# Kernel optimization log

Measured on AMD Instinct MI355X. Metric: run time of the kernel, lower is better.

The kernel has to match this reference:

```python
import jax, jax.numpy as jnp
import numpy as np

S = 2048      # seq_len
H = 32        # num_heads
G = 8         # num_groups (KV heads)
D = 128       # head_dim
HPG = H // G  # heads per group
MODEL = H * D


def setup_inputs() -> dict:
    rng = jax.random.key(0)
    ks = jax.random.split(rng, 6)
    return {
        "query": jax.random.normal(ks[0], (S, H, D), jnp.float32),
        "key":   jax.random.normal(ks[1], (S, G, D), jnp.float32),
        "value": jax.random.normal(ks[2], (S, G, D), jnp.float32),
        "mask":  jnp.zeros((S, S), jnp.float32),
        "w_out": jax.random.normal(ks[3], (MODEL, MODEL), jnp.float32) * (MODEL ** -0.5),
        "b_out": jnp.zeros((MODEL,), jnp.float32),
    }


def reference(query, key, value, mask, w_out, b_out):
    # NOTE: the original torch module prepares `mask` but never applies it to
    # the attention scores; we faithfully reproduce that (mask is unused).
    scale = D ** -0.5
    # [S,H,D] -> [H,S,D] -> [G,HPG,S,D]; head h = g*HPG + i (torch .view split)
    q = query.transpose(1, 0, 2).reshape(G, HPG, S, D)
    k = key.transpose(1, 0, 2)    # [G,S,D]
    v = value.transpose(1, 0, 2)  # [G,S,D]
    scores = jnp.einsum('ghqd,gkd->ghqk', q, k) * scale  # [G,HPG,S,S]
    attn = jax.nn.softmax(scores, axis=-1)
    out = jnp.einsum('ghqk,gkd->ghqd', attn, v)          # [G,HPG,S,D]
    # [G,HPG,S,D] -> [H,S,D] -> [S,H,D] -> [S, H*D]
    out = out.reshape(H, S, D).transpose(1, 0, 2).reshape(S, MODEL)
    out = out @ w_out.T + b_out                           # out_proj (Linear)
    return out.reshape(S, H, D)
```

## Files before the change

kernel.cpp:

```cpp
#include <hip/hip_runtime.h>
#include <hip/hip_bf16.h>
#include <stdint.h>

constexpr int S_ = 2048, H_ = 32, G_ = 8, HPG_ = 4, D_ = 128, MODEL_ = 4096;

typedef __attribute__((ext_vector_type(4))) float f32x4;
typedef __attribute__((ext_vector_type(16))) float f32x16;
typedef __attribute__((ext_vector_type(8))) short bf16x8;
typedef __attribute__((ext_vector_type(4))) short bf16x4;

__device__ inline unsigned short f2bf(float f) {
  unsigned u = __float_as_uint(f);
  u += 0x7FFFu + ((u >> 16) & 1u);
  return (unsigned short)(u >> 16);
}

__device__ inline unsigned cvt_pk_bf16(float lo, float hi) {
  unsigned r;
  asm("v_cvt_pk_bf16_f32 %0, %1, %2" : "=v"(r) : "v"(lo), "v"(hi));
  return r;
}

__device__ inline void gload_lds16(const void* g, void* l) {
  __builtin_amdgcn_global_load_lds(
      (const __attribute__((address_space(1))) unsigned int*)g,
      (__attribute__((address_space(3))) unsigned int*)l,
      16, 0, 0);
}

__global__ __launch_bounds__(256) void cvt_f32_to_bf16(
    const float* __restrict__ in, unsigned short* __restrict__ out, int n4) {
  int i = blockIdx.x * 256 + threadIdx.x;
  if (i < n4) {
    float4 v = reinterpret_cast<const float4*>(in)[i];
    bf16x4 o;
    o[0] = f2bf(v.x); o[1] = f2bf(v.y); o[2] = f2bf(v.z); o[3] = f2bf(v.w);
    reinterpret_cast<bf16x4*>(out)[i] = o;
  }
}

__global__ __launch_bounds__(256) void cvt_k_kernel(
    const float* __restrict__ in, unsigned short* __restrict__ out) {
  int i = blockIdx.x * 256 + threadIdx.x;
  int d4 = i & 31, g = (i >> 5) & 7, s = i >> 8;
  float4 v = reinterpret_cast<const float4*>(in)[i];
  bf16x4 o;
  o[0] = f2bf(v.x); o[1] = f2bf(v.y); o[2] = f2bf(v.z); o[3] = f2bf(v.w);
  reinterpret_cast<bf16x4*>(out)[(g * S_ + s) * 32 + d4] = o;
}

__global__ __launch_bounds__(256) void cvt_v_kernel(
    const float* __restrict__ in, unsigned short* __restrict__ out) {
  __shared__ float t[64][33];
  int s0 = blockIdx.x * 64, d0 = blockIdx.y * 32, g = blockIdx.z;
  int tid = threadIdx.x;
#pragma unroll
  for (int p = 0; p < 2; ++p) {
    int idx = p * 256 + tid;
    int s = idx >> 3, dq = (idx & 7) * 4;
    float4 v = *reinterpret_cast<const float4*>(
        in + ((size_t)(s0 + s) * G_ + g) * D_ + d0 + dq);
    t[s][dq] = v.x; t[s][dq + 1] = v.y; t[s][dq + 2] = v.z; t[s][dq + 3] = v.w;
  }
  __syncthreads();
  int d = tid >> 3, sq = (tid & 7) * 8;
  bf16x8 o;
#pragma unroll
  for (int j = 0; j < 8; ++j) o[j] = f2bf(t[sq + j][d]);
  *reinterpret_cast<bf16x8*>(out + ((size_t)g * D_ + d0 + d) * S_ + s0 + sq) = o;
}

constexpr int QB2 = 128, KVB = 32, NT = S_ / KVB;
constexpr float RTHR = 8.0f;

__global__ __launch_bounds__(256, 2) void attn32_kernel(
    const float* __restrict__ q, const unsigned short* __restrict__ kb,
    const unsigned short* __restrict__ vtb, unsigned short* __restrict__ aout) {
  __shared__ __align__(16) char smem[65536];

  const int qt = blockIdx.x, h = blockIdx.y;
  const int g = h >> 2;
  const int tid = threadIdx.x, w = tid >> 6, lane = tid & 63;
  const int l31 = lane & 31, hi = lane >> 5;

  const float scale2 = 0.12751742354783493f;
  bf16x8 qf[8];
  const int qrow = qt * QB2 + w * 32 + l31;
  {
    const float* qp = q + ((size_t)qrow * H_ + h) * D_;
#pragma unroll
    for (int c = 0; c < 8; ++c) {
      const float* p0 = qp + c * 16 + hi * 8;
      float4 a = *(const float4*)p0;
      float4 b = *(const float4*)(p0 + 4);
      bf16x8 f;
      f[0] = f2bf(a.x * scale2); f[1] = f2bf(a.y * scale2);
      f[2] = f2bf(a.z * scale2); f[3] = f2bf(a.w * scale2);
      f[4] = f2bf(b.x * scale2); f[5] = f2bf(b.y * scale2);
      f[6] = f2bf(b.z * scale2); f[7] = f2bf(b.w * scale2);
      qf[c] = f;
    }
  }

  int ks_kv[2], ks_d[2], vs_d[2], vs_kv[2];
#pragma unroll
  for (int hh = 0; hh < 2; ++hh) {
    int p = w * 1024 + hh * 4096 + lane * 16;
    int kvr = p >> 8;
    ks_kv[hh] = kvr;
    ks_d[hh] = ((p & 255) ^ ((kvr & 7) << 4)) >> 1;
    int dr = p >> 6;
    vs_d[hh] = dr;
    vs_kv[hh] = ((p & 63) ^ (((dr >> 1) & 3) << 4)) >> 1;
  }
  const unsigned short* kg = kb + (size_t)g * S_ * D_;
  const unsigned short* vg = vtb + (size_t)g * D_ * S_;

  auto stage = [&](int t) {
    int kv0 = t * KVB;
    char* Kd = smem + (t & 3) * 16384;
    char* Vd = Kd + 8192;
#pragma unroll
    for (int hh = 0; hh < 2; ++hh) {
      gload_lds16(kg + (size_t)(kv0 + ks_kv[hh]) * D_ + ks_d[hh],
                  Kd + w * 1024 + hh * 4096);
      gload_lds16(vg + (size_t)vs_d[hh] * S_ + kv0 + vs_kv[hh],
                  Vd + w * 1024 + hh * 4096);
    }
  };

  f32x16 of[4];
#pragma unroll
  for (int i = 0; i < 4; ++i) of[i] = (f32x16)0.f;
  float m = -1e30f, l = 0.f;

  auto process = [&](int t) {
    const char* Kd = smem + (t & 3) * 16384;
    const char* Vd = Kd + 8192;

    f32x16 s0 = (f32x16)0.f, s1 = (f32x16)0.f;
    __builtin_amdgcn_s_setprio(1);
#pragma unroll
    for (int c = 0; c < 8; ++c) {
      unsigned off = ((unsigned)(l31 * 256 + c * 32 + hi * 16)) ^
                     ((unsigned)(l31 & 7) << 4);
      bf16x8 kf = *(const bf16x8*)(Kd + off);
      if (c & 1)
        s1 = __builtin_amdgcn_mfma_f32_32x32x16_bf16(kf, qf[c], s1, 0, 0, 0);
      else
        s0 = __builtin_amdgcn_mfma_f32_32x32x16_bf16(kf, qf[c], s0, 0, 0, 0);
    }
    __builtin_amdgcn_s_setprio(0);
    f32x16 sv = s0 + s1;

    float mx8[8];
#pragma unroll
    for (int i = 0; i < 8; ++i) mx8[i] = fmaxf(sv[i], sv[i + 8]);
#pragma unroll
    for (int i = 0; i < 4; ++i) mx8[i] = fmaxf(mx8[i], mx8[i + 4]);
    float tmax = fmaxf(fmaxf(mx8[0], mx8[1]), fmaxf(mx8[2], mx8[3]));
    tmax = fmaxf(tmax, __shfl_xor(tmax, 32));
    if (__any(tmax > m + RTHR)) {
      float mnew = fmaxf(m, tmax);
      float alpha = __builtin_exp2f(m - mnew);
#pragma unroll
      for (int i = 0; i < 4; ++i)
#pragma unroll
        for (int r = 0; r < 16; ++r) of[i][r] *= alpha;
      l *= alpha;
      m = mnew;
    }
    float pv[16], ps[8];
#pragma unroll
    for (int r = 0; r < 16; ++r) pv[r] = __builtin_exp2f(sv[r] - m);
#pragma unroll
    for (int i = 0; i < 8; ++i) ps[i] = pv[i] + pv[i + 8];
#pragma unroll
    for (int i = 0; i < 4; ++i) ps[i] += ps[i + 4];
    float sum = (ps[0] + ps[1]) + (ps[2] + ps[3]);
    sum += __shfl_xor(sum, 32);
    l += sum;

    unsigned pk[8];
#pragma unroll
    for (int b = 0; b < 8; ++b) pk[b] = cvt_pk_bf16(pv[2 * b], pv[2 * b + 1]);
    bf16x8 pf[2];
#pragma unroll
    for (int kc = 0; kc < 2; ++kc) {
      auto sA = __builtin_amdgcn_permlane32_swap(pk[kc * 4 + 0], pk[kc * 4 + 2],
                                                 false, false);
      auto sB = __builtin_amdgcn_permlane32_swap(pk[kc * 4 + 1], pk[kc * 4 + 3],
                                                 false, false);
      unsigned fr[4] = {(unsigned)sA[0], (unsigned)sB[0],
                        (unsigned)sA[1], (unsigned)sB[1]};
      __builtin_memcpy(&pf[kc], fr, 16);
    }

    __builtin_amdgcn_s_setprio(1);
#pragma unroll
    for (int db = 0; db < 4; ++db) {
      int d = db * 32 + l31;
#pragma unroll
      for (int kc = 0; kc < 2; ++kc) {
        unsigned off = ((unsigned)(d * 64 + kc * 32 + hi * 16)) ^
                       ((unsigned)((d >> 1) & 3) << 4);
        bf16x8 vf = *(const bf16x8*)(Vd + off);
        of[db] = __builtin_amdgcn_mfma_f32_32x32x16_bf16(vf, pf[kc], of[db], 0, 0, 0);
      }
    }
    __builtin_amdgcn_s_setprio(0);
  };

  stage(0); stage(1);
  asm volatile("s_waitcnt vmcnt(0)" ::: "memory");
  __builtin_amdgcn_s_barrier();
  stage(2); stage(3);

  for (int t = 0; t < NT; t += 2) {
    process(t);
    process(t + 1);
    asm volatile("s_waitcnt vmcnt(0)" ::: "memory");
    __builtin_amdgcn_s_barrier();
    if (t + 4 < NT) { stage(t + 4); stage(t + 5); }
  }

  __syncthreads();
  float inv = 1.0f / l;
  unsigned short* Ol = (unsigned short*)smem;
  const int ql = w * 32 + l31;
#pragma unroll
  for (int db = 0; db < 4; ++db) {
#pragma unroll
    for (int rp = 0; rp < 8; ++rp) {
      int r0 = rp * 2;
      int d0 = db * 32 + (r0 & 3) + 8 * (r0 >> 2) + 4 * hi;
      unsigned pkv = cvt_pk_bf16(of[db][r0] * inv, of[db][r0 + 1] * inv);
      unsigned off = ((unsigned)(ql * 256 + d0 * 2)) ^ ((unsigned)(ql & 7) << 4);
      *(unsigned*)((char*)Ol + off) = pkv;
    }
  }
  __syncthreads();
  const size_t obase = ((size_t)qt * QB2) * MODEL_ + (size_t)h * D_;
#pragma unroll
  for (int pass = 0; pass < 8; ++pass) {
    int row = pass * 16 + (tid >> 4);
    int c = tid & 15;
    unsigned off = ((unsigned)(row * 256 + c * 16)) ^ ((unsigned)(row & 7) << 4);
    bf16x8 vv = *(const bf16x8*)((char*)Ol + off);
    *(bf16x8*)(aout + obase + (size_t)row * MODEL_ + c * 8) = vv;
  }
}

constexpr int BM = 128, BN = 128, BK = 64;

__global__ __launch_bounds__(256, 2) void gemm_bt_bias(
    const unsigned short* __restrict__ A, const unsigned short* __restrict__ B,
    const float* __restrict__ bias, float* __restrict__ C) {
  __shared__ unsigned short As[BM * BK];
  __shared__ unsigned short Bs[BN * BK];

  const int tid = threadIdx.x;
  const int w = tid >> 6, lane = tid & 63;
  const int wr = w >> 1, wc = w & 1;
  const int r16 = lane & 15, g4 = lane >> 4;
  const int row0 = blockIdx.y * BM, col0 = blockIdx.x * BN;

  f32x4 acc[4][4];
#pragma unroll
  for (int m = 0; m < 4; ++m)
#pragma unroll
    for (int n = 0; n < 4; ++n) acc[m][n] = (f32x4)0.f;

  for (int kt = 0; kt < MODEL_ / BK; ++kt) {
    const int k0 = kt * BK;
    __syncthreads();
#pragma unroll
    for (int j = 0; j < 4; ++j) {
      int chunk = w * 4 + j;
      int sb = chunk * 1024 + lane * 16;
      int srow = sb >> 7;
      int lb = sb ^ ((srow & 7) << 4);
      int kk = (lb & 127) >> 1;
      gload_lds16(A + (size_t)(row0 + srow) * MODEL_ + k0 + kk,
                  (char*)As + chunk * 1024);
      gload_lds16(B + (size_t)(col0 + srow) * MODEL_ + k0 + kk,
                  (char*)Bs + chunk * 1024);
    }
    asm volatile("s_waitcnt vmcnt(0)" ::: "memory");
    __syncthreads();

#pragma unroll
    for (int kc = 0; kc < 2; ++kc) {
      bf16x8 af[4], bfr[4];
#pragma unroll
      for (int m = 0; m < 4; ++m) {
        int row = wr * 64 + m * 16 + r16;
        unsigned off = ((unsigned)(row * 128 + (kc * 32 + g4 * 8) * 2)) ^ ((row & 7) << 4);
        af[m] = *(bf16x8*)((char*)As + off);
      }
#pragma unroll
      for (int n = 0; n < 4; ++n) {
        int row = wc * 64 + n * 16 + r16;
        unsigned off = ((unsigned)(row * 128 + (kc * 32 + g4 * 8) * 2)) ^ ((row & 7) << 4);
        bfr[n] = *(bf16x8*)((char*)Bs + off);
      }
#pragma unroll
      for (int m = 0; m < 4; ++m)
#pragma unroll
        for (int n = 0; n < 4; ++n)
          acc[m][n] = __builtin_amdgcn_mfma_f32_16x16x32_bf16(af[m], bfr[n], acc[m][n], 0, 0, 0);
    }
  }

#pragma unroll
  for (int n = 0; n < 4; ++n) {
    int col = col0 + wc * 64 + n * 16 + r16;
    float bv = bias[col];
#pragma unroll
    for (int m = 0; m < 4; ++m) {
      int rbase = row0 + wr * 64 + m * 16 + g4 * 4;
#pragma unroll
      for (int j = 0; j < 4; ++j)
        C[(size_t)(rbase + j) * MODEL_ + col] = acc[m][n][j] + bv;
    }
  }
}

extern "C" void kernel_launch(void* const* d_in, const int* in_sizes, int n_in,
                              void* d_out, int out_size, void* d_ws, size_t ws_size,
                              hipStream_t stream) {
  const float* q = (const float*)d_in[0];
  const float* k = (const float*)d_in[1];
  const float* v = (const float*)d_in[2];
  const float* w_out = (const float*)d_in[4];
  const float* b_out = (const float*)d_in[5];
  float* out = (float*)d_out;

  unsigned short* attn_bf = (unsigned short*)d_ws;
  unsigned short* xreg = attn_bf + (size_t)S_ * MODEL_;
  unsigned short* k_bf = xreg;
  unsigned short* vt_bf = xreg + (size_t)G_ * S_ * D_;
  unsigned short* w_bf = xreg;
  if (ws_size < ((size_t)S_ * MODEL_ + (size_t)MODEL_ * MODEL_) * 2) return;

  cvt_k_kernel<<<S_ * G_ * D_ / 4 / 256, 256, 0, stream>>>(k, k_bf);
  dim3 vg(S_ / 64, D_ / 32, G_);
  cvt_v_kernel<<<vg, 256, 0, stream>>>(v, vt_bf);

  dim3 ag(S_ / QB2, H_);
  attn32_kernel<<<ag, 256, 0, stream>>>(q, k_bf, vt_bf, attn_bf);

  cvt_f32_to_bf16<<<(MODEL_ * MODEL_ / 4) / 256, 256, 0, stream>>>(
      w_out, w_bf, MODEL_ * MODEL_ / 4);

  dim3 gg(MODEL_ / BN, S_ / BM);
  gemm_bt_bias<<<gg, 256, 0, stream>>>(attn_bf, w_bf, b_out, out);
}
```

Measured before the change: 190.5 us.

## Widen attention KV tile to 64 with double-buffered LDS stages

Raises the KV block per iteration from 32 to 64 keys. Each step now does two score MFMA chains and four PV MFMAs, with a single online-softmax max/rescale check per 64 keys instead of per 32. The LDS layout and XOR swizzles are reworked for 256-byte K rows and 128-byte V^T rows, and the four-slot ring becomes two 32KB buffers. This halves the per-tile softmax and reduction overhead but uses more registers per step and keeps the same total LDS prefetch depth.

Result: slower. 198.1 us (+4.0%).

```diff
diff --git a/kernel.cpp b/kernel.cpp
--- a/kernel.cpp
+++ b/kernel.cpp
@@ -70,7 +70,7 @@
   *reinterpret_cast<bf16x8*>(out + ((size_t)g * D_ + d0 + d) * S_ + s0 + sq) = o;
 }
 
-constexpr int QB2 = 128, KVB = 32, NT = S_ / KVB;
+constexpr int QB2 = 128, KVB = 64, NT2 = S_ / KVB;
 constexpr float RTHR = 8.0f;
 
 __global__ __launch_bounds__(256, 2) void attn32_kernel(
@@ -102,30 +102,30 @@
     }
   }
 
-  int ks_kv[2], ks_d[2], vs_d[2], vs_kv[2];
-#pragma unroll
-  for (int hh = 0; hh < 2; ++hh) {
-    int p = w * 1024 + hh * 4096 + lane * 16;
+  int ks_kv[4], ks_d[4], vs_d[4], vs_kv[4];
+#pragma unroll
+  for (int it = 0; it < 4; ++it) {
+    int p = it * 4096 + w * 1024 + lane * 16;
     int kvr = p >> 8;
-    ks_kv[hh] = kvr;
-    ks_d[hh] = ((p & 255) ^ ((kvr & 7) << 4)) >> 1;
-    int dr = p >> 6;
-    vs_d[hh] = dr;
-    vs_kv[hh] = ((p & 63) ^ (((dr >> 1) & 3) << 4)) >> 1;
+    ks_kv[it] = kvr;
+    ks_d[it] = ((p & 255) ^ ((kvr & 15) << 4)) >> 1;
+    int dr = p >> 7;
+    vs_d[it] = dr;
+    vs_kv[it] = ((p & 127) ^ ((dr & 7) << 4)) >> 1;
   }
   const unsigned short* kg = kb + (size_t)g * S_ * D_;
   const unsigned short* vg = vtb + (size_t)g * D_ * S_;
 
   auto stage = [&](int t) {
     int kv0 = t * KVB;
-    char* Kd = smem + (t & 3) * 16384;
-    char* Vd = Kd + 8192;
-#pragma unroll
-    for (int hh = 0; hh < 2; ++hh) {
-      gload_lds16(kg + (size_t)(kv0 + ks_kv[hh]) * D_ + ks_d[hh],
-                  Kd + w * 1024 + hh * 4096);
-      gload_lds16(vg + (size_t)vs_d[hh] * S_ + kv0 + vs_kv[hh],
-                  Vd + w * 1024 + hh * 4096);
+    char* Kd = smem + (t & 1) * 32768;
+    char* Vd = Kd + 16384;
+#pragma unroll
+    for (int it = 0; it < 4; ++it) {
+      gload_lds16(kg + (size_t)(kv0 + ks_kv[it]) * D_ + ks_d[it],
+                  Kd + it * 4096 + w * 1024);
+      gload_lds16(vg + (size_t)vs_d[it] * S_ + kv0 + vs_kv[it],
+                  Vd + it * 4096 + w * 1024);
     }
   };
 
@@ -135,30 +135,39 @@
   float m = -1e30f, l = 0.f;
 
   auto process = [&](int t) {
-    const char* Kd = smem + (t & 3) * 16384;
-    const char* Vd = Kd + 8192;
+    const char* Kd = smem + (t & 1) * 32768;
+    const char* Vd = Kd + 16384;
 
     f32x16 s0 = (f32x16)0.f, s1 = (f32x16)0.f;
+    f32x16 s2 = (f32x16)0.f, s3 = (f32x16)0.f;
     __builtin_amdgcn_s_setprio(1);
 #pragma unroll
     for (int c = 0; c < 8; ++c) {
-      unsigned off = ((unsigned)(l31 * 256 + c * 32 + hi * 16)) ^
-                     ((unsigned)(l31 & 7) << 4);
-      bf16x8 kf = *(const bf16x8*)(Kd + off);
-      if (c & 1)
-        s1 = __builtin_amdgcn_mfma_f32_32x32x16_bf16(kf, qf[c], s1, 0, 0, 0);
-      else
-        s0 = __builtin_amdgcn_mfma_f32_32x32x16_bf16(kf, qf[c], s0, 0, 0, 0);
+      unsigned off0 = ((unsigned)(l31 * 256 + c * 32 + hi * 16)) ^
+                      ((unsigned)(l31 & 15) << 4);
+      unsigned off1 = ((unsigned)((32 + l31) * 256 + c * 32 + hi * 16)) ^
+                      ((unsigned)(l31 & 15) << 4);
+      bf16x8 kf0 = *(const bf16x8*)(Kd + off0);
+      bf16x8 kf1 = *(const bf16x8*)(Kd + off1);
+      if (c & 1) {
+        s1 = __builtin_amdgcn_mfma_f32_32x32x16_bf16(kf0, qf[c], s1, 0, 0, 0);
+        s3 = __builtin_amdgcn_mfma_f32_32x32x16_bf16(kf1, qf[c], s3, 0, 0, 0);
+      } else {
+        s0 = __builtin_amdgcn_mfma_f32_32x32x16_bf16(kf0, qf[c], s0, 0, 0, 0);
+        s2 = __builtin_amdgcn_mfma_f32_32x32x16_bf16(kf1, qf[c], s2, 0, 0, 0);
+      }
     }
     __builtin_amdgcn_s_setprio(0);
-    f32x16 sv = s0 + s1;
-
-    float mx8[8];
-#pragma unroll
-    for (int i = 0; i < 8; ++i) mx8[i] = fmaxf(sv[i], sv[i + 8]);
-#pragma unroll
-    for (int i = 0; i < 4; ++i) mx8[i] = fmaxf(mx8[i], mx8[i + 4]);
-    float tmax = fmaxf(fmaxf(mx8[0], mx8[1]), fmaxf(mx8[2], mx8[3]));
+    f32x16 sv0 = s0 + s1, sv1 = s2 + s3;
+
+    float mx[16];
+#pragma unroll
+    for (int i = 0; i < 16; ++i) mx[i] = fmaxf(sv0[i], sv1[i]);
+#pragma unroll
+    for (int i = 0; i < 8; ++i) mx[i] = fmaxf(mx[i], mx[i + 8]);
+#pragma unroll
+    for (int i = 0; i < 4; ++i) mx[i] = fmaxf(mx[i], mx[i + 4]);
+    float tmax = fmaxf(fmaxf(mx[0], mx[1]), fmaxf(mx[2], mx[3]));
     tmax = fmaxf(tmax, __shfl_xor(tmax, 32));
     if (__any(tmax > m + RTHR)) {
       float mnew = fmaxf(m, tmax);
@@ -170,30 +179,38 @@
       l *= alpha;
       m = mnew;
     }
-    float pv[16], ps[8];
-#pragma unroll
-    for (int r = 0; r < 16; ++r) pv[r] = __builtin_exp2f(sv[r] - m);
-#pragma unroll
-    for (int i = 0; i < 8; ++i) ps[i] = pv[i] + pv[i + 8];
+    float pv0[16], pv1[16], ps[16];
+#pragma unroll
+    for (int r = 0; r < 16; ++r) pv0[r] = __builtin_exp2f(sv0[r] - m);
+#pragma unroll
+    for (int r = 0; r < 16; ++r) pv1[r] = __builtin_exp2f(sv1[r] - m);
+#pragma unroll
+    for (int i = 0; i < 16; ++i) ps[i] = pv0[i] + pv1[i];
+#pragma unroll
+    for (int i = 0; i < 8; ++i) ps[i] += ps[i + 8];
 #pragma unroll
     for (int i = 0; i < 4; ++i) ps[i] += ps[i + 4];
     float sum = (ps[0] + ps[1]) + (ps[2] + ps[3]);
     sum += __shfl_xor(sum, 32);
     l += sum;
 
-    unsigned pk[8];
-#pragma unroll
-    for (int b = 0; b < 8; ++b) pk[b] = cvt_pk_bf16(pv[2 * b], pv[2 * b + 1]);
-    bf16x8 pf[2];
-#pragma unroll
-    for (int kc = 0; kc < 2; ++kc) {
-      auto sA = __builtin_amdgcn_permlane32_swap(pk[kc * 4 + 0], pk[kc * 4 + 2],
-                                                 false, false);
-      auto sB = __builtin_amdgcn_permlane32_swap(pk[kc * 4 + 1], pk[kc * 4 + 3],
-                                                 false, false);
-      unsigned fr[4] = {(unsigned)sA[0], (unsigned)sB[0],
-                        (unsigned)sA[1], (unsigned)sB[1]};
-      __builtin_memcpy(&pf[kc], fr, 16);
+    bf16x8 pf[4];
+#pragma unroll
+    for (int sl = 0; sl < 2; ++sl) {
+      const float* pp = sl ? pv1 : pv0;
+      unsigned pk[8];
+#pragma unroll
+      for (int b = 0; b < 8; ++b) pk[b] = cvt_pk_bf16(pp[2 * b], pp[2 * b + 1]);
+#pragma unroll
+      for (int kc = 0; kc < 2; ++kc) {
+        auto sA = __builtin_amdgcn_permlane32_swap(pk[kc * 4 + 0], pk[kc * 4 + 2],
+                                                   false, false);
+        auto sB = __builtin_amdgcn_permlane32_swap(pk[kc * 4 + 1], pk[kc * 4 + 3],
+                                                   false, false);
+        unsigned fr[4] = {(unsigned)sA[0], (unsigned)sB[0],
+                          (unsigned)sA[1], (unsigned)sB[1]};
+        __builtin_memcpy(&pf[sl * 2 + kc], fr, 16);
+      }
     }
 
     __builtin_amdgcn_s_setprio(1);
@@ -201,9 +218,9 @@
     for (int db = 0; db < 4; ++db) {
       int d = db * 32 + l31;
 #pragma unroll
-      for (int kc = 0; kc < 2; ++kc) {
-        unsigned off = ((unsigned)(d * 64 + kc * 32 + hi * 16)) ^
-                       ((unsigned)((d >> 1) & 3) << 4);
+      for (int kc = 0; kc < 4; ++kc) {
+        unsigned off = ((unsigned)(d * 128 + kc * 32 + hi * 16)) ^
+                       ((unsigned)(d & 7) << 4);
         bf16x8 vf = *(const bf16x8*)(Vd + off);
         of[db] = __builtin_amdgcn_mfma_f32_32x32x16_bf16(vf, pf[kc], of[db], 0, 0, 0);
       }
@@ -211,17 +228,16 @@
     __builtin_amdgcn_s_setprio(0);
   };
 
-  stage(0); stage(1);
+  stage(0);
   asm volatile("s_waitcnt vmcnt(0)" ::: "memory");
   __builtin_amdgcn_s_barrier();
-  stage(2); stage(3);
-
-  for (int t = 0; t < NT; t += 2) {
+  stage(1);
+
+  for (int t = 0; t < NT2; ++t) {
     process(t);
-    process(t + 1);
     asm volatile("s_waitcnt vmcnt(0)" ::: "memory");
     __builtin_amdgcn_s_barrier();
-    if (t + 4 < NT) { stage(t + 4); stage(t + 5); }
+    if (t + 2 < NT2) stage(t + 2);
   }
 
   __syncthreads();
```

## Split attention KV range across two wave groups and merge partial softmax

Applied to the files above, without the earlier changes.

Each attention block now runs 512 threads, with two groups of four waves each processing half of the KV sequence for the same 128 query rows. The partial outputs and running max/sum are merged through shared memory at the end. Staging also drops from a 4-deep to a 2-deep buffer per group, with new LDS swizzles for K and V and a single MFMA accumulator chain. The aim is more waves in flight per CU to hide latency. In exchange it pays for a final merge with extra barriers and LDS traffic, and launch_bounds(512,4) may put pressure on registers.

Result: slower. 281.2 us (+47.6%).

```diff
diff --git a/kernel.cpp b/kernel.cpp
--- a/kernel.cpp
+++ b/kernel.cpp
@@ -70,23 +70,24 @@
   *reinterpret_cast<bf16x8*>(out + ((size_t)g * D_ + d0 + d) * S_ + s0 + sq) = o;
 }
 
-constexpr int QB2 = 128, KVB = 32, NT = S_ / KVB;
+constexpr int QB2 = 128, KVB = 32, NTG = 1024 / KVB;
 constexpr float RTHR = 8.0f;
 
-__global__ __launch_bounds__(256, 2) void attn32_kernel(
+__global__ __launch_bounds__(512, 4) void attn32_kernel(
     const float* __restrict__ q, const unsigned short* __restrict__ kb,
     const unsigned short* __restrict__ vtb, unsigned short* __restrict__ aout) {
-  __shared__ __align__(16) char smem[65536];
+  __shared__ __align__(16) char smem[66560];
 
   const int qt = blockIdx.x, h = blockIdx.y;
   const int g = h >> 2;
   const int tid = threadIdx.x, w = tid >> 6, lane = tid & 63;
   const int l31 = lane & 31, hi = lane >> 5;
+  const int gsel = w >> 2, wq = w & 3;
 
   const float scale2 = 0.12751742354783493f;
   bf16x8 qf[8];
-  const int qrow = qt * QB2 + w * 32 + l31;
   {
+    const int qrow = qt * QB2 + wq * 32 + l31;
     const float* qp = q + ((size_t)qrow * H_ + h) * D_;
 #pragma unroll
     for (int c = 0; c < 8; ++c) {
@@ -102,30 +103,31 @@
     }
   }
 
-  int ks_kv[2], ks_d[2], vs_d[2], vs_kv[2];
-#pragma unroll
-  for (int hh = 0; hh < 2; ++hh) {
-    int p = w * 1024 + hh * 4096 + lane * 16;
+  int kvK[2], dK[2], dV[2], kvV[2];
+#pragma unroll
+  for (int j = 0; j < 2; ++j) {
+    int p = (wq * 2 + j) * 1024 + lane * 16;
     int kvr = p >> 8;
-    ks_kv[hh] = kvr;
-    ks_d[hh] = ((p & 255) ^ ((kvr & 7) << 4)) >> 1;
-    int dr = p >> 6;
-    vs_d[hh] = dr;
-    vs_kv[hh] = ((p & 63) ^ (((dr >> 1) & 3) << 4)) >> 1;
+    kvK[j] = kvr;
+    dK[j] = ((p & 255) ^ ((kvr & 15) << 4)) >> 1;
+    int R = p >> 8;
+    int il = (p & 255) ^ ((R & 7) << 4);
+    dV[j] = R * 4 + (il >> 6);
+    kvV[j] = (il & 63) >> 1;
   }
   const unsigned short* kg = kb + (size_t)g * S_ * D_;
   const unsigned short* vg = vtb + (size_t)g * D_ * S_;
+  const int kvbase = gsel * 1024;
 
   auto stage = [&](int t) {
-    int kv0 = t * KVB;
-    char* Kd = smem + (t & 3) * 16384;
-    char* Vd = Kd + 8192;
-#pragma unroll
-    for (int hh = 0; hh < 2; ++hh) {
-      gload_lds16(kg + (size_t)(kv0 + ks_kv[hh]) * D_ + ks_d[hh],
-                  Kd + w * 1024 + hh * 4096);
-      gload_lds16(vg + (size_t)vs_d[hh] * S_ + kv0 + vs_kv[hh],
-                  Vd + w * 1024 + hh * 4096);
+    int kv0 = kvbase + t * KVB;
+    char* base = smem + (gsel * 2 + (t & 1)) * 16384;
+#pragma unroll
+    for (int j = 0; j < 2; ++j) {
+      gload_lds16(kg + (size_t)(kv0 + kvK[j]) * D_ + dK[j],
+                  base + (wq * 2 + j) * 1024);
+      gload_lds16(vg + (size_t)dV[j] * S_ + kv0 + kvV[j],
+                  base + 8192 + (wq * 2 + j) * 1024);
     }
   };
 
@@ -134,31 +136,33 @@
   for (int i = 0; i < 4; ++i) of[i] = (f32x16)0.f;
   float m = -1e30f, l = 0.f;
 
-  auto process = [&](int t) {
-    const char* Kd = smem + (t & 3) * 16384;
+  stage(0);
+  asm volatile("s_waitcnt vmcnt(0)" ::: "memory");
+  __builtin_amdgcn_s_barrier();
+
+  for (int t = 0; t < NTG; ++t) {
+    if (t + 1 < NTG) stage(t + 1);
+
+    const char* Kd = smem + (gsel * 2 + (t & 1)) * 16384;
     const char* Vd = Kd + 8192;
 
-    f32x16 s0 = (f32x16)0.f, s1 = (f32x16)0.f;
+    f32x16 sv = (f32x16)0.f;
     __builtin_amdgcn_s_setprio(1);
 #pragma unroll
     for (int c = 0; c < 8; ++c) {
-      unsigned off = ((unsigned)(l31 * 256 + c * 32 + hi * 16)) ^
-                     ((unsigned)(l31 & 7) << 4);
+      unsigned off = (unsigned)(l31 * 256) +
+                     (((unsigned)(c * 32 + hi * 16)) ^ ((unsigned)(l31 & 15) << 4));
       bf16x8 kf = *(const bf16x8*)(Kd + off);
-      if (c & 1)
-        s1 = __builtin_amdgcn_mfma_f32_32x32x16_bf16(kf, qf[c], s1, 0, 0, 0);
-      else
-        s0 = __builtin_amdgcn_mfma_f32_32x32x16_bf16(kf, qf[c], s0, 0, 0, 0);
+      sv = __builtin_amdgcn_mfma_f32_32x32x16_bf16(kf, qf[c], sv, 0, 0, 0);
     }
     __builtin_amdgcn_s_setprio(0);
-    f32x16 sv = s0 + s1;
-
-    float mx8[8];
-#pragma unroll
-    for (int i = 0; i < 8; ++i) mx8[i] = fmaxf(sv[i], sv[i + 8]);
-#pragma unroll
-    for (int i = 0; i < 4; ++i) mx8[i] = fmaxf(mx8[i], mx8[i + 4]);
-    float tmax = fmaxf(fmaxf(mx8[0], mx8[1]), fmaxf(mx8[2], mx8[3]));
+
+    float mx[8];
+#pragma unroll
+    for (int i = 0; i < 8; ++i) mx[i] = fmaxf(sv[i], sv[i + 8]);
+#pragma unroll
+    for (int i = 0; i < 4; ++i) mx[i] = fmaxf(mx[i], mx[i + 4]);
+    float tmax = fmaxf(fmaxf(mx[0], mx[1]), fmaxf(mx[2], mx[3]));
     tmax = fmaxf(tmax, __shfl_xor(tmax, 32));
     if (__any(tmax > m + RTHR)) {
       float mnew = fmaxf(m, tmax);
@@ -199,51 +203,72 @@
     __builtin_amdgcn_s_setprio(1);
 #pragma unroll
     for (int db = 0; db < 4; ++db) {
-      int d = db * 32 + l31;
+      int R = db * 8 + (l31 >> 2);
+      unsigned lg = (unsigned)((l31 & 3) * 64);
 #pragma unroll
       for (int kc = 0; kc < 2; ++kc) {
-        unsigned off = ((unsigned)(d * 64 + kc * 32 + hi * 16)) ^
-                       ((unsigned)((d >> 1) & 3) << 4);
+        unsigned off = (unsigned)(R * 256) +
+                       ((lg + (unsigned)(kc * 32 + hi * 16)) ^ ((unsigned)(R & 7) << 4));
         bf16x8 vf = *(const bf16x8*)(Vd + off);
         of[db] = __builtin_amdgcn_mfma_f32_32x32x16_bf16(vf, pf[kc], of[db], 0, 0, 0);
       }
     }
     __builtin_amdgcn_s_setprio(0);
-  };
-
-  stage(0); stage(1);
-  asm volatile("s_waitcnt vmcnt(0)" ::: "memory");
-  __builtin_amdgcn_s_barrier();
-  stage(2); stage(3);
-
-  for (int t = 0; t < NT; t += 2) {
-    process(t);
-    process(t + 1);
+
     asm volatile("s_waitcnt vmcnt(0)" ::: "memory");
     __builtin_amdgcn_s_barrier();
-    if (t + 4 < NT) { stage(t + 4); stage(t + 5); }
-  }
-
+  }
+
+  float* O1 = (float*)smem;
+  float* ml = (float*)(smem + 65536);
+  if (w >= 4) {
+    float* reg = O1 + (w - 4) * 4096;
+#pragma unroll
+    for (int db = 0; db < 4; ++db)
+#pragma unroll
+      for (int r = 0; r < 16; ++r) {
+        int dd = db * 32 + (r & 3) + 8 * (r >> 2) + 4 * hi;
+        reg[dd * 32 + l31] = of[db][r];
+      }
+    if (!hi) { ml[wq * 64 + l31 * 2] = m; ml[wq * 64 + l31 * 2 + 1] = l; }
+  }
   __syncthreads();
-  float inv = 1.0f / l;
+  float inv = 0.f;
+  if (w < 4) {
+    float m1 = ml[wq * 64 + l31 * 2], l1 = ml[wq * 64 + l31 * 2 + 1];
+    float mf = fmaxf(m, m1);
+    float a0 = __builtin_exp2f(m - mf), a1 = __builtin_exp2f(m1 - mf);
+    inv = 1.0f / (l * a0 + l1 * a1);
+    const float* reg = O1 + wq * 4096;
+#pragma unroll
+    for (int db = 0; db < 4; ++db)
+#pragma unroll
+      for (int r = 0; r < 16; ++r) {
+        int dd = db * 32 + (r & 3) + 8 * (r >> 2) + 4 * hi;
+        of[db][r] = of[db][r] * a0 + reg[dd * 32 + l31] * a1;
+      }
+  }
+  __syncthreads();
+
   unsigned short* Ol = (unsigned short*)smem;
-  const int ql = w * 32 + l31;
-#pragma unroll
-  for (int db = 0; db < 4; ++db) {
-#pragma unroll
-    for (int rp = 0; rp < 8; ++rp) {
-      int r0 = rp * 2;
-      int d0 = db * 32 + (r0 & 3) + 8 * (r0 >> 2) + 4 * hi;
-      unsigned pkv = cvt_pk_bf16(of[db][r0] * inv, of[db][r0 + 1] * inv);
-      unsigned off = ((unsigned)(ql * 256 + d0 * 2)) ^ ((unsigned)(ql & 7) << 4);
-      *(unsigned*)((char*)Ol + off) = pkv;
-    }
+  if (w < 4) {
+    const int ql = wq * 32 + l31;
+#pragma unroll
+    for (int db = 0; db < 4; ++db)
+#pragma unroll
+      for (int rp = 0; rp < 8; ++rp) {
+        int r0 = rp * 2;
+        int d0 = db * 32 + (r0 & 3) + 8 * (r0 >> 2) + 4 * hi;
+        unsigned pkv = cvt_pk_bf16(of[db][r0] * inv, of[db][r0 + 1] * inv);
+        unsigned off = ((unsigned)(ql * 256 + d0 * 2)) ^ ((unsigned)(ql & 7) << 4);
+        *(unsigned*)((char*)Ol + off) = pkv;
+      }
   }
   __syncthreads();
   const size_t obase = ((size_t)qt * QB2) * MODEL_ + (size_t)h * D_;
 #pragma unroll
-  for (int pass = 0; pass < 8; ++pass) {
-    int row = pass * 16 + (tid >> 4);
+  for (int pass = 0; pass < 4; ++pass) {
+    int row = pass * 32 + (tid >> 4);
     int c = tid & 15;
     unsigned off = ((unsigned)(row * 256 + c * 16)) ^ ((unsigned)(row & 7) << 4);
     bf16x8 vv = *(const bf16x8*)((char*)Ol + off);
@@ -348,7 +373,7 @@
   cvt_v_kernel<<<vg, 256, 0, stream>>>(v, vt_bf);
 
   dim3 ag(S_ / QB2, H_);
-  attn32_kernel<<<ag, 256, 0, stream>>>(q, k_bf, vt_bf, attn_bf);
+  attn32_kernel<<<ag, 512, 0, stream>>>(q, k_bf, vt_bf, attn_bf);
 
   cvt_f32_to_bf16<<<(MODEL_ * MODEL_ / 4) / 256, 256, 0, stream>>>(
       w_out, w_bf, MODEL_ * MODEL_ / 4);
```
